# Kernel tuning notes

Measured on AMD Instinct MI355X. Metric: run time of the kernel, lower is better.

The kernel has to match this reference:

```python
import jax, jax.numpy as jnp
import numpy as np

NB, T, NS, NC = 32, 256, 64, 32
NSC = NS + NC


def setup_inputs() -> dict:
    key = jax.random.key(0)
    k1, k2, k3, k4, k5, k6 = jax.random.split(key, 6)
    Qr = jax.random.normal(k1, (NB, T, NSC, NSC), jnp.float32)
    # SPD cost matrices (example does Q = Q.mT @ Q); add ridge so Quu is well conditioned
    Q = jnp.einsum('btki,btkj->btij', Qr, Qr) / NSC + 0.5 * jnp.eye(NSC, dtype=jnp.float32)
    p = jax.random.normal(k2, (NB, T, NSC), jnp.float32)
    A = jnp.eye(NS, dtype=jnp.float32)[None] + 0.01 * jax.random.normal(k3, (NB, NS, NS), jnp.float32)
    B = 0.1 * jax.random.normal(k4, (NB, NS, NC), jnp.float32)
    c1 = 0.01 * jax.random.normal(k5, (NB, NS), jnp.float32)
    x_init = jax.random.normal(k6, (NB, NS), jnp.float32)
    return {'Q': Q, 'p': p, 'A': A, 'B': B, 'c1': c1, 'x_init': x_init}


def _lqr(Q, p, A, B, c1, x_init):
    ns = A.shape[-1]
    F = jnp.concatenate([A, B], axis=-1)  # [nb, ns, nsc]

    # ---- backward Riccati recursion (t = T-1 .. 0) ----
    def bwd(carry, inp):
        V, v = carry              # [nb,ns,ns], [nb,ns]
        Qt, pt = inp              # [nb,nsc,nsc], [nb,nsc]
        FtV = jnp.einsum('bsj,bsk->bjk', F, V)          # F^T V  [nb,nsc,ns]
        Qh = Qt + FtV @ F                               # Q + F^T V F
        qh = pt + jnp.einsum('bjk,bk->bj', FtV, c1) + jnp.einsum('bsj,bs->bj', F, v)
        Qxx = Qh[:, :ns, :ns]
        Qxu = Qh[:, :ns, ns:]
        Qux = Qh[:, ns:, :ns]
        Quu = Qh[:, ns:, ns:]
        qx, qu = qh[:, :ns], qh[:, ns:]
        K = -jnp.linalg.solve(Quu, Qux)                 # -Quu^{-1} Qux  [nb,nc,ns]
        kk = -jnp.linalg.solve(Quu, qu[..., None])[..., 0]
        Kt = jnp.swapaxes(K, -1, -2)
        Vn = Qxx + Qxu @ K + Kt @ Qux + Kt @ (Quu @ K)
        vn = qx + jnp.einsum('bsu,bu->bs', Qxu, kk) \
            + jnp.einsum('bus,bu->bs', K, qu + jnp.einsum('buw,bw->bu', Quu, kk))
        return (Vn, vn), (K, kk)

    nb = Q.shape[0]
    V0 = jnp.zeros((nb, ns, ns), Q.dtype)
    v0 = jnp.zeros((nb, ns), Q.dtype)
    Qs = jnp.swapaxes(Q, 0, 1)   # [T,nb,nsc,nsc]
    ps = jnp.swapaxes(p, 0, 1)
    _, (Ks, ks) = jax.lax.scan(bwd, (V0, v0), (jnp.flip(Qs, 0), jnp.flip(ps, 0)))
    Ks = jnp.flip(Ks, 0)
    ks = jnp.flip(ks, 0)

    # ---- forward rollout (t = 0 .. T-1) ----
    def fwd(x, inp):
        K, kk, Qt, pt = inp
        u = jnp.einsum('bus,bs->bu', K, x) + kk
        tau = jnp.concatenate([x, u], axis=-1)
        c = 0.5 * jnp.einsum('bi,bij,bj->b', tau, Qt, tau) + jnp.einsum('bi,bi->b', pt, tau)
        xn = jnp.einsum('bij,bj->bi', A, x) + jnp.einsum('bij,bj->bi', B, u) + c1
        return xn, (x, u, c)

    _, (xs, us, cs) = jax.lax.scan(fwd, x_init, (Ks, ks, Qs, ps))
    x = jnp.swapaxes(xs, 0, 1)   # [nb,T,ns]
    u = jnp.swapaxes(us, 0, 1)   # [nb,T,nc]
    cost = jnp.sum(cs, axis=0)   # [nb]
    return x, u, cost


def reference(Q, p, A, B, c1, x_init):
    return _lqr(Q, p, A, B, c1, x_init)
```

## Files before the change

### kernel.cpp

```cpp
#include <hip/hip_runtime.h>

#define NB 32
#define T 256
#define NS 64
#define NC 32
#define NSC 96

typedef short bf16x8 __attribute__((ext_vector_type(8)));
typedef float f32x4  __attribute__((ext_vector_type(4)));

#define COMP(v,i) ((i)==0?(v).x:((i)==1?(v).y:((i)==2?(v).z:(v).w)))

static __device__ __forceinline__ float dot4(float4 a, float4 b){
    return fmaf(a.x,b.x, fmaf(a.y,b.y, fmaf(a.z,b.z, a.w*b.w)));
}
static __device__ __forceinline__ unsigned short f2bf(float x){
    unsigned int u = __float_as_uint(x);
    u += 0x7FFFu + ((u >> 16) & 1u);
    return (unsigned short)(u >> 16);
}
static __device__ __forceinline__ float bf2f(unsigned short h){
    return __uint_as_float(((unsigned int)h) << 16);
}

__device__ __align__(16) float g_KtG[(size_t)NB*T*NS*NC];
__device__ __align__(16) float g_kkG[(size_t)NB*T*NC];

#define BROW 72

__device__ __forceinline__ void p2geom(int tix, int& i0, int& j0, int& osel){
    if (tix < 16)      { i0 = (tix & 3)*16;              j0 = (tix >> 2)*16;        osel = 0; }
    else if (tix < 24) { const int q = tix-16; i0 = (q & 3)*16;  j0 = 64 + (q >> 2)*16; osel = 1; }
    else               { const int q = tix-24; i0 = 64 + (q & 1)*16; j0 = 64 + (q >> 1)*16; osel = 2; }
}

#define P1TILE(tix) { \
    const int s0 = ((tix) & 3) * 16, j0 = ((tix) >> 2) * 16; \
    f32x4 c = {0.f, 0.f, 0.f, 0.f}; \
    _Pragma("unroll") \
    for (int kc = 0; kc < 2; ++kc) { \
        const int ch = (kc*4 + lk) * 8; \
        const bf16x8 ah = *(const bf16x8*)&Vbh[(s0+lm)*BROW + ch]; \
        const bf16x8 al = *(const bf16x8*)&Vbl[(s0+lm)*BROW + ch]; \
        const bf16x8 bh = *(const bf16x8*)&Fth[(j0+lm)*BROW + ch]; \
        const bf16x8 bl = *(const bf16x8*)&Ftl[(j0+lm)*BROW + ch]; \
        c = __builtin_amdgcn_mfma_f32_16x16x32_bf16(ah, bh, c, 0, 0, 0); \
        c = __builtin_amdgcn_mfma_f32_16x16x32_bf16(ah, bl, c, 0, 0, 0); \
        c = __builtin_amdgcn_mfma_f32_16x16x32_bf16(al, bh, c, 0, 0, 0); \
    } \
    ushort4 hv, lv; float rm_; \
    hv.x = f2bf(c[0]); rm_ = c[0] - bf2f(hv.x); lv.x = f2bf(rm_); \
    hv.y = f2bf(c[1]); rm_ = c[1] - bf2f(hv.y); lv.y = f2bf(rm_); \
    hv.z = f2bf(c[2]); rm_ = c[2] - bf2f(hv.z); lv.z = f2bf(rm_); \
    hv.w = f2bf(c[3]); rm_ = c[3] - bf2f(hv.w); lv.w = f2bf(rm_); \
    const int ui = (j0+lm)*BROW + s0 + lk*4; \
    *(ushort4*)&Wth[ui] = hv; \
    *(ushort4*)&Wtl[ui] = lv; \
}

#define P2TILE(cin, tix) { \
    int i0_, j0_, os_; p2geom((tix), i0_, j0_, os_); \
    f32x4 c = cin; \
    _Pragma("unroll") \
    for (int kc = 0; kc < 2; ++kc) { \
        const int ch = (kc*4 + lk) * 8; \
        const bf16x8 ah = *(const bf16x8*)&Fth[(i0_+lm)*BROW + ch]; \
        const bf16x8 al = *(const bf16x8*)&Ftl[(i0_+lm)*BROW + ch]; \
        const bf16x8 bh = *(const bf16x8*)&Wth[(j0_+lm)*BROW + ch]; \
        const bf16x8 bl = *(const bf16x8*)&Wtl[(j0_+lm)*BROW + ch]; \
        c = __builtin_amdgcn_mfma_f32_16x16x32_bf16(ah, bh, c, 0, 0, 0); \
        c = __builtin_amdgcn_mfma_f32_16x16x32_bf16(ah, bl, c, 0, 0, 0); \
        c = __builtin_amdgcn_mfma_f32_16x16x32_bf16(al, bh, c, 0, 0, 0); \
    } \
    _Pragma("unroll") \
    for (int r = 0; r < 4; ++r) { \
        const int i_ = i0_ + lk*4 + r, j_ = j0_ + lm; \
        if (os_ == 0) { V[i_][j_] = c[r]; } \
        else if (os_ == 1) { Qxu[i_][j_-64] = c[r]; } \
        else { \
            const int wr_ = i_ - 64, u_ = j_ - 64; \
            Maug[wr_][u_] = c[r]; QuuC[wr_][u_] = c[r]; \
            if (wr_ == 0) { prow[0][u_] = c[r]; prow[0][32+u_] = (u_ == 0) ? 1.f : 0.f; } \
            if (u_ == 0) pfac[0][wr_] = c[r]; \
        } \
    } \
}

__global__ __launch_bounds__(512)
void lqr_bwd(const float* __restrict__ Qg_, const float* __restrict__ pg_,
             const float* __restrict__ Ag_, const float* __restrict__ Bg_,
             const float* __restrict__ c1g_, const float* __restrict__ x0g_,
             float* __restrict__ outc)
{
    __shared__ __align__(16) float V[64][68];
    __shared__ __align__(16) unsigned short Vbh[64*BROW];
    __shared__ __align__(16) unsigned short Vbl[64*BROW];
    __shared__ __align__(16) unsigned short Fth[96*BROW];
    __shared__ __align__(16) unsigned short Ftl[96*BROW];
    __shared__ __align__(16) unsigned short Wth[96*BROW];
    __shared__ __align__(16) unsigned short Wtl[96*BROW];
    __shared__ __align__(16) float Qxu[64][36];
    __shared__ __align__(16) float QuuC[32][36];
    __shared__ __align__(16) float Maug[32][68];
    __shared__ __align__(16) float Kt[64][36];
    __shared__ __align__(16) float prow[2][64];
    __shared__ __align__(16) float pfac[2][32];
    __shared__ __align__(16) float qh[96];
    __shared__ __align__(16) float gv[64];
    __shared__ __align__(16) float hbuf[32];
    __shared__ __align__(16) float c1l[64];
    __shared__ __align__(16) float vl[64];
    __shared__ __align__(16) float kkl[32];
    __shared__ __align__(16) float x0l[64];
    __shared__ float wpart[8];
    __shared__ float wAcc;

    float (*Rt)[36] = reinterpret_cast<float (*)[36]>(&Wth[0]);

    const int tid = threadIdx.x;
    const int b   = blockIdx.x;
    const int w   = tid >> 6;
    const int lm  = tid & 15;
    const int lk  = (tid & 63) >> 4;

    const float* Qg = Qg_ + (size_t)b*T*NSC*NSC;
    const float* pg = pg_ + (size_t)b*T*NSC;
    const float* Ag = Ag_ + (size_t)b*NS*NS;
    const float* Bg = Bg_ + (size_t)b*NS*NC;
    float* KtG = g_KtG + (size_t)b*T*NS*NC;
    float* kkG = g_kkG + (size_t)b*T*NC;

    for (int e = tid; e < 96*64; e += 512) {
        const int j = e >> 6, s = e & 63;
        const float x = (j < 64) ? Ag[s*64 + j] : Bg[s*32 + (j-64)];
        const unsigned short h = f2bf(x);
        Fth[j*BROW + s] = h;
        Ftl[j*BROW + s] = f2bf(x - bf2f(h));
    }
    for (int e = tid; e < 64*BROW; e += 512) { Vbh[e] = 0; Vbl[e] = 0; }
    for (int e = tid; e < 64*68; e += 512) ((float*)V)[e] = 0.f;
    if (tid < 64) { c1l[tid] = c1g_[b*64+tid]; vl[tid] = 0.f; x0l[tid] = x0g_[b*64+tid]; }
    if (tid == 0) wAcc = 0.f;
    __syncthreads();

    const int wq  = tid >> 4;
    const int gjq = tid & 15, gj0 = gjq * 4;

    const int p2s = (w < 4) ? w*4 : 16 + (w-4)*3;
    const int p2n = (w < 4) ? 4 : 3;

    for (int t = T-1; t >= 0; --t) {
        const float* Qt = Qg + (size_t)t*NSC*NSC;
        const float* pt = pg + (size_t)t*NSC;

        f32x4 qt0, qt1, qt2, qt3;
        {
            int i0, j0, os;
            p2geom(p2s+0, i0, j0, os);
            const float* s0p = Qt + (size_t)(i0 + lk*4)*96 + j0 + lm;
            qt0[0]=s0p[0]; qt0[1]=s0p[96]; qt0[2]=s0p[192]; qt0[3]=s0p[288];
            p2geom(p2s+1, i0, j0, os);
            const float* s1p = Qt + (size_t)(i0 + lk*4)*96 + j0 + lm;
            qt1[0]=s1p[0]; qt1[1]=s1p[96]; qt1[2]=s1p[192]; qt1[3]=s1p[288];
            p2geom(p2s+2, i0, j0, os);
            const float* s2p = Qt + (size_t)(i0 + lk*4)*96 + j0 + lm;
            qt2[0]=s2p[0]; qt2[1]=s2p[96]; qt2[2]=s2p[192]; qt2[3]=s2p[288];
            if (p2n == 4) {
                p2geom(p2s+3, i0, j0, os);
                const float* s3p = Qt + (size_t)(i0 + lk*4)*96 + j0 + lm;
                qt3[0]=s3p[0]; qt3[1]=s3p[96]; qt3[2]=s3p[192]; qt3[3]=s3p[288];
            } else { qt3 = qt0; }
        }

        {
            const int l = tid >> 3, g = tid & 7;
            const int k0 = g * 8;
            float d = dot4(*(const float4*)&V[l][k0],   *(const float4*)&c1l[k0])
                    + dot4(*(const float4*)&V[l][k0+4], *(const float4*)&c1l[k0+4]);
            d += __shfl_xor(d, 1); d += __shfl_xor(d, 2); d += __shfl_xor(d, 4);
            if (g == 0) gv[l] = d + vl[l];
            float term = (g == 0) ? c1l[l]*(0.5f*d + vl[l]) : 0.f;
            term += __shfl_xor(term, 8); term += __shfl_xor(term, 16); term += __shfl_xor(term, 32);
            if ((tid & 63) == 0) wpart[w] = term;
        }
        __syncthreads();

        if (tid < 384) {
            const int j = tid >> 2, g = tid & 3;
            const int s0 = g * 16;
            const bf16x8 h0 = *(const bf16x8*)&Fth[j*BROW + s0];
            const bf16x8 l0 = *(const bf16x8*)&Ftl[j*BROW + s0];
            const bf16x8 h1 = *(const bf16x8*)&Fth[j*BROW + s0 + 8];
            const bf16x8 l1 = *(const bf16x8*)&Ftl[j*BROW + s0 + 8];
            float s = 0.f;
            #pragma unroll
            for (int i = 0; i < 8; ++i) {
                s = fmaf(bf2f((unsigned short)h0[i]) + bf2f((unsigned short)l0[i]), gv[s0+i],   s);
                s = fmaf(bf2f((unsigned short)h1[i]) + bf2f((unsigned short)l1[i]), gv[s0+8+i], s);
            }
            s += __shfl_xor(s, 1); s += __shfl_xor(s, 2);
            if (g == 0) qh[j] = pt[j] + s;
        } else if (tid == 448) {
            float s = 0.f;
            #pragma unroll
            for (int i = 0; i < 8; ++i) s += wpart[i];
            wAcc += s;
        }
        __syncthreads();

        {
            const int st = w * 3;
            P1TILE(st+0)
            P1TILE(st+1)
            P1TILE(st+2)
        }
        __syncthreads();

        P2TILE(qt0, p2s+0)
        P2TILE(qt1, p2s+1)
        P2TILE(qt2, p2s+2)
        if (p2n == 4) { P2TILE(qt3, p2s+3) }
        __syncthreads();

        {
            float4 m;
            if (gjq < 8) m = *(const float4*)&Maug[wq][gj0];
            else {
                const int base = gj0 - 32;
                m.x = (base+0==wq)?1.f:0.f; m.y = (base+1==wq)?1.f:0.f;
                m.z = (base+2==wq)?1.f:0.f; m.w = (base+3==wq)?1.f:0.f;
            }
            #pragma unroll
            for (int k = 0; k < 32; ++k) {
                const int par = k & 1, nxt = par ^ 1;
                const float pinv = 1.0f / prow[par][k];
                const float4 pr = *(const float4*)&prow[par][gj0];
                if (wq == k) {
                    m.x = pr.x*pinv; m.y = pr.y*pinv; m.z = pr.z*pinv; m.w = pr.w*pinv;
                } else {
                    const float fac = pfac[par][wq]*pinv;
                    m.x = fmaf(-fac,pr.x,m.x); m.y = fmaf(-fac,pr.y,m.y);
                    m.z = fmaf(-fac,pr.z,m.z); m.w = fmaf(-fac,pr.w,m.w);
                }
                if (k < 31) {
                    if (wq == k+1) *(float4*)&prow[nxt][gj0] = m;
                    if (((k+1)>>2) == gjq) pfac[nxt][wq] = COMP(m,(k+1)&3);
                } else if (gjq >= 8) {
                    *(float4*)&Maug[wq][gj0] = m;
                }
                __syncthreads();
            }
        }

        {
            const int i = tid >> 3, u0 = (tid & 7) * 4;
            float a0=0,a1=0,a2=0,a3=0;
            #pragma unroll
            for (int w4 = 0; w4 < 8; ++w4) {
                const int wb = w4*4;
                const float4 q4 = *(const float4*)&Qxu[i][wb];
                const float4 m0 = *(const float4*)&Maug[u0+0][32+wb];
                const float4 m1 = *(const float4*)&Maug[u0+1][32+wb];
                const float4 m2 = *(const float4*)&Maug[u0+2][32+wb];
                const float4 m3 = *(const float4*)&Maug[u0+3][32+wb];
                a0 -= dot4(q4,m0); a1 -= dot4(q4,m1);
                a2 -= dot4(q4,m2); a3 -= dot4(q4,m3);
            }
            const float4 kt4 = make_float4(a0,a1,a2,a3);
            *(float4*)&Kt[i][u0] = kt4;
            *(float4*)&KtG[(size_t)t*2048 + i*32 + u0] = kt4;
            if (tid < 32) {
                float ka = 0.f;
                #pragma unroll
                for (int w4 = 0; w4 < 8; ++w4)
                    ka -= dot4(*(const float4*)&Maug[tid][32+w4*4], *(const float4*)&qh[64+w4*4]);
                kkl[tid] = ka;
                kkG[t*32 + tid] = ka;
            }
        }
        __syncthreads();

        {
            const int j = tid >> 3, u0 = (tid & 7) * 4;
            const float4 qx4 = *(const float4*)&Qxu[j][u0];
            float g0=qx4.x, g1=qx4.y, g2=qx4.z, g3=qx4.w;
            #pragma unroll
            for (int w4 = 0; w4 < 8; ++w4) {
                const int wb = w4*4;
                const float4 k4 = *(const float4*)&Kt[j][wb];
                g0 += dot4(*(const float4*)&QuuC[u0+0][wb], k4);
                g1 += dot4(*(const float4*)&QuuC[u0+1][wb], k4);
                g2 += dot4(*(const float4*)&QuuC[u0+2][wb], k4);
                g3 += dot4(*(const float4*)&QuuC[u0+3][wb], k4);
            }
            *(float4*)&Rt[j][u0] = make_float4(g0,g1,g2,g3);
            if (tid < 32) {
                float h = qh[64+tid];
                #pragma unroll
                for (int w4 = 0; w4 < 8; ++w4)
                    h += dot4(*(const float4*)&QuuC[tid][w4*4], *(const float4*)&kkl[w4*4]);
                hbuf[tid] = h;
            }
        }
        __syncthreads();

        {
            const int jj = tid & 31, i0 = (tid >> 5) * 4;
            float aA[4], aB[4];
            #pragma unroll
            for (int r = 0; r < 4; ++r) { aA[r] = V[i0+r][jj]; aB[r] = V[i0+r][32+jj]; }
            #pragma unroll
            for (int u4 = 0; u4 < 8; ++u4) {
                const int ub = u4*4;
                const float4 kja = *(const float4*)&Kt[jj][ub];
                const float4 kjb = *(const float4*)&Kt[32+jj][ub];
                const float4 rja = *(const float4*)&Rt[jj][ub];
                const float4 rjb = *(const float4*)&Rt[32+jj][ub];
                #pragma unroll
                for (int r = 0; r < 4; ++r) {
                    const float4 xi = *(const float4*)&Qxu[i0+r][ub];
                    const float4 ki = *(const float4*)&Kt[i0+r][ub];
                    aA[r] += dot4(xi,kja) + dot4(ki,rja);
                    aB[r] += dot4(xi,kjb) + dot4(ki,rjb);
                }
            }
            #pragma unroll
            for (int r = 0; r < 4; ++r) { V[i0+r][jj] = aA[r]; V[i0+r][32+jj] = aB[r]; }
        }
        __syncthreads();

        if (tid < 256) {
            const int a = tid >> 4, bq = tid & 15;
            if (a < bq) {
                float4 t1[4], t2[4];
                #pragma unroll
                for (int r = 0; r < 4; ++r) {
                    t1[r] = *(const float4*)&V[4*a+r][4*bq];
                    t2[r] = *(const float4*)&V[4*bq+r][4*a];
                }
                #pragma unroll
                for (int r = 0; r < 4; ++r) {
                    float4 o, p;
                    o.x = 0.5f*(COMP(t1[r],0)+COMP(t2[0],r));
                    o.y = 0.5f*(COMP(t1[r],1)+COMP(t2[1],r));
                    o.z = 0.5f*(COMP(t1[r],2)+COMP(t2[2],r));
                    o.w = 0.5f*(COMP(t1[r],3)+COMP(t2[3],r));
                    p.x = 0.5f*(COMP(t2[r],0)+COMP(t1[0],r));
                    p.y = 0.5f*(COMP(t2[r],1)+COMP(t1[1],r));
                    p.z = 0.5f*(COMP(t2[r],2)+COMP(t1[2],r));
                    p.w = 0.5f*(COMP(t2[r],3)+COMP(t1[3],r));
                    *(float4*)&V[4*a+r][4*bq] = o;
                    *(float4*)&V[4*bq+r][4*a] = p;
                    ushort4 oh, ol, ph, pl;
                    oh.x=f2bf(o.x); ol.x=f2bf(o.x-bf2f(oh.x));
                    oh.y=f2bf(o.y); ol.y=f2bf(o.y-bf2f(oh.y));
                    oh.z=f2bf(o.z); ol.z=f2bf(o.z-bf2f(oh.z));
                    oh.w=f2bf(o.w); ol.w=f2bf(o.w-bf2f(oh.w));
                    ph.x=f2bf(p.x); pl.x=f2bf(p.x-bf2f(ph.x));
                    ph.y=f2bf(p.y); pl.y=f2bf(p.y-bf2f(ph.y));
                    ph.z=f2bf(p.z); pl.z=f2bf(p.z-bf2f(ph.z));
                    ph.w=f2bf(p.w); pl.w=f2bf(p.w-bf2f(ph.w));
                    *(ushort4*)&Vbh[(4*a+r)*BROW + 4*bq] = oh;
                    *(ushort4*)&Vbl[(4*a+r)*BROW + 4*bq] = ol;
                    *(ushort4*)&Vbh[(4*bq+r)*BROW + 4*a] = ph;
                    *(ushort4*)&Vbl[(4*bq+r)*BROW + 4*a] = pl;
                }
            } else if (a == bq) {
                float4 t1[4];
                #pragma unroll
                for (int r = 0; r < 4; ++r) t1[r] = *(const float4*)&V[4*a+r][4*a];
                #pragma unroll
                for (int r = 0; r < 4; ++r) {
                    float4 o;
                    o.x = 0.5f*(COMP(t1[r],0)+COMP(t1[0],r));
                    o.y = 0.5f*(COMP(t1[r],1)+COMP(t1[1],r));
                    o.z = 0.5f*(COMP(t1[r],2)+COMP(t1[2],r));
                    o.w = 0.5f*(COMP(t1[r],3)+COMP(t1[3],r));
                    *(float4*)&V[4*a+r][4*a] = o;
                    ushort4 oh, ol;
                    oh.x=f2bf(o.x); ol.x=f2bf(o.x-bf2f(oh.x));
                    oh.y=f2bf(o.y); ol.y=f2bf(o.y-bf2f(oh.y));
                    oh.z=f2bf(o.z); ol.z=f2bf(o.z-bf2f(oh.z));
                    oh.w=f2bf(o.w); ol.w=f2bf(o.w-bf2f(oh.w));
                    *(ushort4*)&Vbh[(4*a+r)*BROW + 4*a] = oh;
                    *(ushort4*)&Vbl[(4*a+r)*BROW + 4*a] = ol;
                }
            }
        } else if (tid < 320) {
            const int l = tid - 256;
            float vv = qh[l];
            #pragma unroll
            for (int u4 = 0; u4 < 8; ++u4) {
                vv += dot4(*(const float4*)&Qxu[l][u4*4], *(const float4*)&kkl[u4*4]);
                vv += dot4(*(const float4*)&Kt[l][u4*4],  *(const float4*)&hbuf[u4*4]);
            }
            vl[l] = vv;
        } else if (tid < 352) {
            const int u = tid - 320;
            float r = kkl[u]*(hbuf[u] + qh[64+u]);
            r += __shfl_xor(r,16); r += __shfl_xor(r,8); r += __shfl_xor(r,4);
            r += __shfl_xor(r,2);  r += __shfl_xor(r,1);
            if (u == 0) wAcc += 0.5f*r;
        }
        __syncthreads();
    }

    if (tid < 64) {
        float rd = 0.f;
        #pragma unroll
        for (int k4 = 0; k4 < 16; ++k4)
            rd += dot4(*(const float4*)&V[tid][k4*4], *(const float4*)&x0l[k4*4]);
        float ps = x0l[tid]*(0.5f*rd + vl[tid]);
        ps += __shfl_xor(ps,32); ps += __shfl_xor(ps,16); ps += __shfl_xor(ps,8);
        ps += __shfl_xor(ps,4);  ps += __shfl_xor(ps,2);  ps += __shfl_xor(ps,1);
        if (tid == 0) outc[b] = wAcc + ps;
    }
}

__global__ __launch_bounds__(256)
void lqr_fwd(const float* __restrict__ Ag_, const float* __restrict__ Bg_,
             const float* __restrict__ c1g_, const float* __restrict__ x0g_,
             float* __restrict__ outx, float* __restrict__ outu)
{
    __shared__ __align__(16) float At[64][68];
    __shared__ __align__(16) float Bt[32][68];
    __shared__ __align__(16) float KtL[64][36];
    __shared__ float xl[64], ul[32], cl[64], kl[32], xnb[64];

    const int tid = threadIdx.x;
    const int b = blockIdx.x;

    const float* KtG = g_KtG + (size_t)b*T*NS*NC;
    const float* kkG = g_kkG + (size_t)b*T*NC;

    for (int e = tid; e < NS*NS; e += 256) At[e&63][e>>6] = Ag_[(size_t)b*4096 + e];
    for (int e = tid; e < NS*NC; e += 256) Bt[e&31][e>>5] = Bg_[(size_t)b*2048 + e];
    if (tid < 64) { xl[tid] = x0g_[b*64 + tid]; cl[tid] = c1g_[b*64 + tid]; }

    {
        const int i1 = tid*4, i2 = 1024 + tid*4;
        const float4 a = *(const float4*)&KtG[i1];
        const float4 c = *(const float4*)&KtG[i2];
        *(float4*)&KtL[i1>>5][i1&31] = a;
        *(float4*)&KtL[i2>>5][i2&31] = c;
        if (tid < 32) kl[tid] = kkG[tid];
    }
    __syncthreads();

    float4 g0, g1; float kn = 0.f;
    for (int t = 0; t < T; ++t) {
        if (t+1 < T) {
            g0 = *(const float4*)&KtG[(size_t)(t+1)*2048 + tid*4];
            g1 = *(const float4*)&KtG[(size_t)(t+1)*2048 + 1024 + tid*4];
            if (tid < 32) kn = kkG[(t+1)*32 + tid];
        }

        if (tid < 64) outx[((size_t)b*T + t)*64 + tid] = xl[tid];
        if (tid < 128) {
            const int u = tid >> 2, sp = tid & 3, s0 = sp*16;
            float r = 0.f;
            #pragma unroll
            for (int i = 0; i < 16; ++i) r = fmaf(KtL[s0+i][u], xl[s0+i], r);
            r += __shfl_xor(r, 1); r += __shfl_xor(r, 2);
            if (sp == 0) {
                const float uu = r + kl[u];
                ul[u] = uu;
                outu[((size_t)b*T + t)*32 + u] = uu;
            }
        }
        __syncthreads();

        {
            const int o = tid >> 2, sp = tid & 3;
            float r = 0.f;
            #pragma unroll
            for (int i = 0; i < 16; ++i) { const int j = sp*16 + i; r = fmaf(At[j][o], xl[j], r); }
            #pragma unroll
            for (int i = 0; i < 8; ++i)  { const int w2 = sp*8 + i; r = fmaf(Bt[w2][o], ul[w2], r); }
            r += __shfl_xor(r, 1); r += __shfl_xor(r, 2);
            if (sp == 0) xnb[o] = r + cl[o];
        }
        __syncthreads();

        if (tid < 64) xl[tid] = xnb[tid];
        if (t+1 < T) {
            const int i1 = tid*4, i2 = 1024 + tid*4;
            *(float4*)&KtL[i1>>5][i1&31] = g0;
            *(float4*)&KtL[i2>>5][i2&31] = g1;
            if (tid < 32) kl[tid] = kn;
        }
        __syncthreads();
    }
}

extern "C" void kernel_launch(void* const* d_in, const int* in_sizes, int n_in,
                              void* d_out, int out_size, void* d_ws, size_t ws_size,
                              hipStream_t stream)
{
    const float* Q  = (const float*)d_in[0];
    const float* p  = (const float*)d_in[1];
    const float* A  = (const float*)d_in[2];
    const float* B  = (const float*)d_in[3];
    const float* c1 = (const float*)d_in[4];
    const float* x0 = (const float*)d_in[5];

    float* outx = (float*)d_out;
    float* outu = outx + (size_t)NB*T*NS;
    float* outc = outu + (size_t)NB*T*NC;

    lqr_bwd<<<NB, 512, 0, stream>>>(Q, p, A, B, c1, x0, outc);
    lqr_fwd<<<NB, 256, 0, stream>>>(A, B, c1, x0, outx, outu);
}
```

Measured before the change: 5.488 ms.

## Move K, R and V-update matmuls in Riccati step onto split-bf16 MFMA

Replaces three scalar fp32 dot-product stages in the backward Riccati loop (K = -Qxu·Minv, R = K·Quu + Qxu, V += Qxu·Kt + K·Rt) with 16x16x32 bf16 MFMA tiles using hi/lo bf16 splits to keep near-fp32 accuracy. Adds shared buffers for bf16 hi/lo copies of Qxu, Kt, Minv and Quu, plus a conversion pass over Minv with an extra barrier. R is stored only as a single bf16 (no lo part), and the K·R term uses only the hi product, so precision is lower than before. Each step is serial per block, so cutting per-step latency is the goal.

```diff
diff --git a/kernel.cpp b/kernel.cpp
--- a/kernel.cpp
+++ b/kernel.cpp
@@ -27,6 +27,7 @@
 __device__ __align__(16) float g_kkG[(size_t)NB*T*NC];
 
 #define BROW 72
+#define SR32 36
 
 __device__ __forceinline__ void p2geom(int tix, int& i0, int& j0, int& osel){
     if (tix < 16)      { i0 = (tix & 3)*16;              j0 = (tix >> 2)*16;        osel = 0; }
@@ -76,10 +77,18 @@
     for (int r = 0; r < 4; ++r) { \
         const int i_ = i0_ + lk*4 + r, j_ = j0_ + lm; \
         if (os_ == 0) { V[i_][j_] = c[r]; } \
-        else if (os_ == 1) { Qxu[i_][j_-64] = c[r]; } \
-        else { \
+        else if (os_ == 1) { \
+            const int u_ = j_ - 64; \
+            Qxu[i_][u_] = c[r]; \
+            const unsigned short h_ = f2bf(c[r]); \
+            Qxuh[i_*SR32 + u_] = h_; \
+            Qxul[i_*SR32 + u_] = f2bf(c[r] - bf2f(h_)); \
+        } else { \
             const int wr_ = i_ - 64, u_ = j_ - 64; \
             Maug[wr_][u_] = c[r]; QuuC[wr_][u_] = c[r]; \
+            const unsigned short h_ = f2bf(c[r]); \
+            Quuh[wr_*SR32 + u_] = h_; \
+            Quul[wr_*SR32 + u_] = f2bf(c[r] - bf2f(h_)); \
             if (wr_ == 0) { prow[0][u_] = c[r]; prow[0][32+u_] = (u_ == 0) ? 1.f : 0.f; } \
             if (u_ == 0) pfac[0][wr_] = c[r]; \
         } \
@@ -102,9 +111,13 @@
     __shared__ __align__(16) float Qxu[64][36];
     __shared__ __align__(16) float QuuC[32][36];
     __shared__ __align__(16) float Maug[32][68];
-    __shared__ __align__(16) float Kt[64][36];
     __shared__ __align__(16) float prow[2][64];
     __shared__ __align__(16) float pfac[2][32];
+    __shared__ __align__(16) unsigned short Qxuh[64*SR32], Qxul[64*SR32];
+    __shared__ __align__(16) unsigned short Kth[64*SR32],  Ktl[64*SR32];
+    __shared__ __align__(16) unsigned short Minvh[32*SR32], Minvl[32*SR32];
+    __shared__ __align__(16) unsigned short Quuh[32*SR32],  Quul[32*SR32];
+    __shared__ __align__(16) unsigned short Rth[64*SR32];
     __shared__ __align__(16) float qh[96];
     __shared__ __align__(16) float gv[64];
     __shared__ __align__(16) float hbuf[32];
@@ -114,8 +127,6 @@
     __shared__ __align__(16) float x0l[64];
     __shared__ float wpart[8];
     __shared__ float wAcc;
-
-    float (*Rt)[36] = reinterpret_cast<float (*)[36]>(&Wth[0]);
 
     const int tid = threadIdx.x;
     const int b   = blockIdx.x;
@@ -253,22 +264,35 @@
         }
 
         {
-            const int i = tid >> 3, u0 = (tid & 7) * 4;
-            float a0=0,a1=0,a2=0,a3=0;
-            #pragma unroll
-            for (int w4 = 0; w4 < 8; ++w4) {
-                const int wb = w4*4;
-                const float4 q4 = *(const float4*)&Qxu[i][wb];
-                const float4 m0 = *(const float4*)&Maug[u0+0][32+wb];
-                const float4 m1 = *(const float4*)&Maug[u0+1][32+wb];
-                const float4 m2 = *(const float4*)&Maug[u0+2][32+wb];
-                const float4 m3 = *(const float4*)&Maug[u0+3][32+wb];
-                a0 -= dot4(q4,m0); a1 -= dot4(q4,m1);
-                a2 -= dot4(q4,m2); a3 -= dot4(q4,m3);
-            }
-            const float4 kt4 = make_float4(a0,a1,a2,a3);
-            *(float4*)&Kt[i][u0] = kt4;
-            *(float4*)&KtG[(size_t)t*2048 + i*32 + u0] = kt4;
+            const int e0 = tid * 2;
+            const int u = e0 >> 5, w0 = e0 & 31;
+            const float m0 = Maug[u][32+w0], m1 = Maug[u][32+w0+1];
+            const unsigned short h0 = f2bf(m0), h1 = f2bf(m1);
+            Minvh[u*SR32 + w0]   = h0;  Minvl[u*SR32 + w0]   = f2bf(m0 - bf2f(h0));
+            Minvh[u*SR32 + w0+1] = h1;  Minvl[u*SR32 + w0+1] = f2bf(m1 - bf2f(h1));
+        }
+        __syncthreads();
+
+        {
+            const int i0 = (w & 3)*16, u0 = (w >> 2)*16;
+            const int ch = lk*8;
+            f32x4 c = {0.f,0.f,0.f,0.f};
+            const bf16x8 ah = *(const bf16x8*)&Qxuh[(i0+lm)*SR32 + ch];
+            const bf16x8 al = *(const bf16x8*)&Qxul[(i0+lm)*SR32 + ch];
+            const bf16x8 bh = *(const bf16x8*)&Minvh[(u0+lm)*SR32 + ch];
+            const bf16x8 bl = *(const bf16x8*)&Minvl[(u0+lm)*SR32 + ch];
+            c = __builtin_amdgcn_mfma_f32_16x16x32_bf16(ah, bh, c, 0, 0, 0);
+            c = __builtin_amdgcn_mfma_f32_16x16x32_bf16(ah, bl, c, 0, 0, 0);
+            c = __builtin_amdgcn_mfma_f32_16x16x32_bf16(al, bh, c, 0, 0, 0);
+            #pragma unroll
+            for (int r = 0; r < 4; ++r) {
+                const int i_ = i0 + lk*4 + r, u_ = u0 + lm;
+                const float kv = -c[r];
+                KtG[(size_t)t*2048 + i_*32 + u_] = kv;
+                const unsigned short h = f2bf(kv);
+                Kth[i_*SR32 + u_] = h;
+                Ktl[i_*SR32 + u_] = f2bf(kv - bf2f(h));
+            }
             if (tid < 32) {
                 float ka = 0.f;
                 #pragma unroll
@@ -281,19 +305,21 @@
         __syncthreads();
 
         {
-            const int j = tid >> 3, u0 = (tid & 7) * 4;
-            const float4 qx4 = *(const float4*)&Qxu[j][u0];
-            float g0=qx4.x, g1=qx4.y, g2=qx4.z, g3=qx4.w;
-            #pragma unroll
-            for (int w4 = 0; w4 < 8; ++w4) {
-                const int wb = w4*4;
-                const float4 k4 = *(const float4*)&Kt[j][wb];
-                g0 += dot4(*(const float4*)&QuuC[u0+0][wb], k4);
-                g1 += dot4(*(const float4*)&QuuC[u0+1][wb], k4);
-                g2 += dot4(*(const float4*)&QuuC[u0+2][wb], k4);
-                g3 += dot4(*(const float4*)&QuuC[u0+3][wb], k4);
-            }
-            *(float4*)&Rt[j][u0] = make_float4(g0,g1,g2,g3);
+            const int j0 = (w & 3)*16, u0 = (w >> 2)*16;
+            const int ch = lk*8;
+            f32x4 c;
+            #pragma unroll
+            for (int r = 0; r < 4; ++r) c[r] = Qxu[j0 + lk*4 + r][u0 + lm];
+            const bf16x8 ah = *(const bf16x8*)&Kth[(j0+lm)*SR32 + ch];
+            const bf16x8 al = *(const bf16x8*)&Ktl[(j0+lm)*SR32 + ch];
+            const bf16x8 bh = *(const bf16x8*)&Quuh[(u0+lm)*SR32 + ch];
+            const bf16x8 bl = *(const bf16x8*)&Quul[(u0+lm)*SR32 + ch];
+            c = __builtin_amdgcn_mfma_f32_16x16x32_bf16(ah, bh, c, 0, 0, 0);
+            c = __builtin_amdgcn_mfma_f32_16x16x32_bf16(ah, bl, c, 0, 0, 0);
+            c = __builtin_amdgcn_mfma_f32_16x16x32_bf16(al, bh, c, 0, 0, 0);
+            #pragma unroll
+            for (int r = 0; r < 4; ++r)
+                Rth[(j0 + lk*4 + r)*SR32 + u0 + lm] = f2bf(c[r]);
             if (tid < 32) {
                 float h = qh[64+tid];
                 #pragma unroll
@@ -304,28 +330,26 @@
         }
         __syncthreads();
 
-        {
-            const int jj = tid & 31, i0 = (tid >> 5) * 4;
-            float aA[4], aB[4];
-            #pragma unroll
-            for (int r = 0; r < 4; ++r) { aA[r] = V[i0+r][jj]; aB[r] = V[i0+r][32+jj]; }
-            #pragma unroll
-            for (int u4 = 0; u4 < 8; ++u4) {
-                const int ub = u4*4;
-                const float4 kja = *(const float4*)&Kt[jj][ub];
-                const float4 kjb = *(const float4*)&Kt[32+jj][ub];
-                const float4 rja = *(const float4*)&Rt[jj][ub];
-                const float4 rjb = *(const float4*)&Rt[32+jj][ub];
-                #pragma unroll
-                for (int r = 0; r < 4; ++r) {
-                    const float4 xi = *(const float4*)&Qxu[i0+r][ub];
-                    const float4 ki = *(const float4*)&Kt[i0+r][ub];
-                    aA[r] += dot4(xi,kja) + dot4(ki,rja);
-                    aB[r] += dot4(xi,kjb) + dot4(ki,rjb);
-                }
-            }
-            #pragma unroll
-            for (int r = 0; r < 4; ++r) { V[i0+r][jj] = aA[r]; V[i0+r][32+jj] = aB[r]; }
+        #pragma unroll
+        for (int half = 0; half < 2; ++half) {
+            const int tx = w + half*8;
+            const int i0 = (tx & 3)*16, j0 = (tx >> 2)*16;
+            const int ch = lk*8;
+            f32x4 c;
+            #pragma unroll
+            for (int r = 0; r < 4; ++r) c[r] = V[i0 + lk*4 + r][j0 + lm];
+            const bf16x8 ah  = *(const bf16x8*)&Qxuh[(i0+lm)*SR32 + ch];
+            const bf16x8 al  = *(const bf16x8*)&Qxul[(i0+lm)*SR32 + ch];
+            const bf16x8 bh  = *(const bf16x8*)&Kth[(j0+lm)*SR32 + ch];
+            const bf16x8 bl  = *(const bf16x8*)&Ktl[(j0+lm)*SR32 + ch];
+            const bf16x8 a2h = *(const bf16x8*)&Kth[(i0+lm)*SR32 + ch];
+            const bf16x8 b2h = *(const bf16x8*)&Rth[(j0+lm)*SR32 + ch];
+            c = __builtin_amdgcn_mfma_f32_16x16x32_bf16(ah,  bh,  c, 0, 0, 0);
+            c = __builtin_amdgcn_mfma_f32_16x16x32_bf16(ah,  bl,  c, 0, 0, 0);
+            c = __builtin_amdgcn_mfma_f32_16x16x32_bf16(al,  bh,  c, 0, 0, 0);
+            c = __builtin_amdgcn_mfma_f32_16x16x32_bf16(a2h, b2h, c, 0, 0, 0);
+            #pragma unroll
+            for (int r = 0; r < 4; ++r) V[i0 + lk*4 + r][j0 + lm] = c[r];
         }
         __syncthreads();
 
@@ -390,9 +414,16 @@
             const int l = tid - 256;
             float vv = qh[l];
             #pragma unroll
-            for (int u4 = 0; u4 < 8; ++u4) {
+            for (int u4 = 0; u4 < 8; ++u4)
                 vv += dot4(*(const float4*)&Qxu[l][u4*4], *(const float4*)&kkl[u4*4]);
-                vv += dot4(*(const float4*)&Kt[l][u4*4],  *(const float4*)&hbuf[u4*4]);
+            #pragma unroll
+            for (int cg = 0; cg < 4; ++cg) {
+                const bf16x8 h8 = *(const bf16x8*)&Kth[l*SR32 + cg*8];
+                const bf16x8 l8 = *(const bf16x8*)&Ktl[l*SR32 + cg*8];
+                #pragma unroll
+                for (int i = 0; i < 8; ++i)
+                    vv = fmaf(bf2f((unsigned short)h8[i]) + bf2f((unsigned short)l8[i]),
+                              hbuf[cg*8+i], vv);
             }
             vl[l] = vv;
         } else if (tid < 352) {
```

New measurement: 4.916 ms. 10.4% less time.
